# Kernel optimization log

Hardware: AMD Instinct MI355X
Metric: run time of the kernel (lower is better)

Reference implementation:

```python
import jax, jax.numpy as jnp
import numpy as np

N_NODES = 100000
N_EDGES = 3200000

def setup_inputs() -> dict:
    key = jax.random.key(0)
    ks = jax.random.split(key, 6)
    x = jax.random.normal(ks[0], (N_NODES, 128), dtype=jnp.float32)
    edge_index = jax.random.randint(ks[1], (2, N_EDGES), 0, N_NODES, dtype=jnp.int64)
    W1 = jax.random.normal(ks[2], (128, 64), dtype=jnp.float32) * 0.05
    b1 = jnp.zeros((64,), dtype=jnp.float32)
    W2 = jax.random.normal(ks[3], (64, 64), dtype=jnp.float32) * 0.05
    b2 = jnp.zeros((64,), dtype=jnp.float32)
    Wf = jax.random.normal(ks[4], (64, 40), dtype=jnp.float32) * 0.05
    bf = jnp.zeros((40,), dtype=jnp.float32)
    return {"x": x, "edge_index": edge_index, "W1": W1, "b1": b1,
            "W2": W2, "b2": b2, "Wf": Wf, "bf": bf}

def _gcn_graph(edge_index, n_nodes):
    # Add self loops (PyG GCNConv default), compute symmetric norm.
    loop = jnp.arange(n_nodes, dtype=edge_index.dtype)
    src = jnp.concatenate([edge_index[0], loop])
    dst = jnp.concatenate([edge_index[1], loop])
    deg = jax.ops.segment_sum(jnp.ones_like(dst, dtype=jnp.float32), dst,
                              num_segments=n_nodes)
    dinv = jnp.where(deg > 0, jax.lax.rsqrt(deg), 0.0)
    norm = dinv[src] * dinv[dst]  # [E+N]
    return src, dst, norm

def _gcn_layer(x, W, b, src, dst, norm, n_nodes):
    h = x @ W                     # transform first (as PyG GCNConv)
    msg = h[src] * norm[:, None]  # gather + scale
    agg = jax.ops.segment_sum(msg, dst, num_segments=n_nodes)  # scatter-sum
    return agg + b

def reference(x, edge_index, W1, b1, W2, b2, Wf, bf):
    n = x.shape[0]
    src, dst, norm = _gcn_graph(edge_index, n)
    h = jax.nn.relu(_gcn_layer(x, W1, b1, src, dst, norm, n))
    h = jax.nn.relu(_gcn_layer(h, W2, b2, src, dst, norm, n))
    logits = h @ Wf + bf
    return jax.nn.log_softmax(logits, axis=1)
```

## Files before the change

### kernel.cpp

```cpp
#include <hip/hip_runtime.h>
#include <hip/hip_fp16.h>
#include <cstdint>
#include <cstddef>
#include <cmath>


#define T1  4096
#define BSH 7
#define CAP 6144

typedef _Float16 half8 __attribute__((ext_vector_type(8)));
typedef float f32x4 __attribute__((ext_vector_type(4)));
typedef float f32x2 __attribute__((ext_vector_type(2)));

__global__ __launch_bounds__(1024) void k_prep(const float* __restrict__ W1,
        const float* __restrict__ W2, const float* __restrict__ Wf,
        int* __restrict__ cursor1, uint4* __restrict__ W1fr,
        uint4* __restrict__ W2fr, uint4* __restrict__ Wffr, int NB) {
    int t = threadIdx.x;
    for (int i = t; i < NB; i += 1024) cursor1[i] = i * CAP;
    if (t < 64) {
        int r16 = t & 15, kg = t >> 4;
        #pragma unroll
        for (int ct = 0; ct < 4; ++ct)
            #pragma unroll
            for (int kt = 0; kt < 4; ++kt) {
                half8 h;
                #pragma unroll
                for (int j = 0; j < 8; ++j)
                    h[j] = (_Float16)W1[(kt * 32 + kg * 8 + j) * 64 + ct * 16 + r16];
                W1fr[(ct * 4 + kt) * 64 + t] = *(uint4*)&h;
            }
        #pragma unroll
        for (int ct = 0; ct < 4; ++ct)
            #pragma unroll
            for (int kt = 0; kt < 2; ++kt) {
                half8 h;
                #pragma unroll
                for (int j = 0; j < 8; ++j)
                    h[j] = (_Float16)W2[(kt * 32 + kg * 8 + j) * 64 + ct * 16 + r16];
                W2fr[(ct * 2 + kt) * 64 + t] = *(uint4*)&h;
            }
        #pragma unroll
        for (int ct = 0; ct < 3; ++ct)
            #pragma unroll
            for (int kt = 0; kt < 2; ++kt) {
                int col = ct * 16 + r16;
                half8 h;
                #pragma unroll
                for (int j = 0; j < 8; ++j)
                    h[j] = (col < 40) ? (_Float16)Wf[(kt * 32 + kg * 8 + j) * 40 + col]
                                      : (_Float16)0.f;
                Wffr[(ct * 2 + kt) * 64 + t] = *(uint4*)&h;
            }
    }
}

__global__ __launch_bounds__(256) void k_pass1(const int* __restrict__ src,
        const int* __restrict__ dst, int* __restrict__ cursor1,
        unsigned int* __restrict__ tmp, int E, int NB) {
    __shared__ unsigned int pack[T1];
    __shared__ unsigned short bkt[T1];
    __shared__ int h[1024], hs_[1024], gbase[1024];
    __shared__ int wtot[4];
    int t = threadIdx.x;
    for (int i = t; i < 1024; i += 256) h[i] = 0;
    __syncthreads();
    int base = blockIdx.x * T1;
    int n = min(T1, E - base);
    int nv4 = n >> 2, rem = n & 3;
    unsigned int pk[16];
    int bl[16];
    #pragma unroll
    for (int i = 0; i < 4; ++i) {
        int g = i * 256 + t;
        if (g < nv4) {
            int4 s4 = ((const int4*)(src + base))[g];
            int4 d4 = ((const int4*)(dst + base))[g];
            int b0 = d4.x >> BSH;
            pk[4*i]   = (unsigned)s4.x | ((unsigned)(d4.x & 127) << 17);
            bl[4*i]   = (b0 << 13) | atomicAdd(&h[b0], 1);
            int b1 = d4.y >> BSH;
            pk[4*i+1] = (unsigned)s4.y | ((unsigned)(d4.y & 127) << 17);
            bl[4*i+1] = (b1 << 13) | atomicAdd(&h[b1], 1);
            int b2 = d4.z >> BSH;
            pk[4*i+2] = (unsigned)s4.z | ((unsigned)(d4.z & 127) << 17);
            bl[4*i+2] = (b2 << 13) | atomicAdd(&h[b2], 1);
            int b3 = d4.w >> BSH;
            pk[4*i+3] = (unsigned)s4.w | ((unsigned)(d4.w & 127) << 17);
            bl[4*i+3] = (b3 << 13) | atomicAdd(&h[b3], 1);
        } else {
            bl[4*i] = bl[4*i+1] = bl[4*i+2] = bl[4*i+3] = -1;
        }
    }
    unsigned int pk_r = 0; int bl_r = -1;
    if (t < rem) {
        int idx = nv4 * 4 + t;
        int s_ = src[base + idx], d = dst[base + idx];
        int b = d >> BSH;
        pk_r = (unsigned)s_ | ((unsigned)(d & 127) << 17);
        bl_r = (b << 13) | atomicAdd(&h[b], 1);
    }
    __syncthreads();
    {
        int b0 = 4 * t;
        int e0 = h[b0], e1 = h[b0+1], e2 = h[b0+2], e3 = h[b0+3];
        int s1 = e0 + e1, s2 = s1 + e2, s3 = s2 + e3;
        int lane = t & 63, wv = t >> 6;
        int vv = s3;
        #pragma unroll
        for (int o = 1; o < 64; o <<= 1) {
            int u = __shfl_up(vv, o, 64);
            if (lane >= o) vv += u;
        }
        if (lane == 63) wtot[wv] = vv;
        __syncthreads();
        int off = 0;
        #pragma unroll
        for (int w = 0; w < 4; ++w) off += (w < wv) ? wtot[w] : 0;
        int excl = off + vv - s3;
        hs_[b0]   = excl + e0;
        hs_[b0+1] = excl + s1;
        hs_[b0+2] = excl + s2;
        hs_[b0+3] = excl + s3;
    }
    __syncthreads();
    for (int i = t; i < NB; i += 256)
        gbase[i] = h[i] ? atomicAdd(&cursor1[i], h[i]) : 0;
    __syncthreads();
    #pragma unroll
    for (int i = 0; i < 16; ++i) {
        if (bl[i] >= 0) {
            int b = bl[i] >> 13, lo = bl[i] & 8191;
            int slot = hs_[b] - h[b] + lo;
            pack[slot] = pk[i];
            bkt[slot]  = (unsigned short)b;
        }
    }
    if (bl_r >= 0) {
        int b = bl_r >> 13, lo = bl_r & 8191;
        int slot = hs_[b] - h[b] + lo;
        pack[slot] = pk_r;
        bkt[slot]  = (unsigned short)b;
    }
    __syncthreads();
    for (int s_ = t; s_ < n; s_ += 256) {
        int b = bkt[s_];
        tmp[gbase[b] + (s_ - (hs_[b] - h[b]))] = pack[s_];
    }
}

__global__ __launch_bounds__(512) void k_p2x(const unsigned int* __restrict__ tmp,
        const int* __restrict__ cursor1, int2* __restrict__ rcp,
        int* __restrict__ csrc, float* __restrict__ dinv,
        const float* __restrict__ x, const uint4* __restrict__ W1fr,
        unsigned int* __restrict__ hs, int N) {
    __shared__ int c[8][128], cur[8][128];
    __shared__ float sdinv[128];
    __shared__ int wsum;
    int t = threadIdx.x, b = blockIdx.x;
    int wv = t >> 6;
    for (int i = t; i < 1024; i += 512) ((int*)c)[i] = 0;
    __syncthreads();
    int s0 = b * CAP, s1 = cursor1[b];
    int n = s1 - s0;
    int nv4 = n >> 2, rem = n & 3;
    const uint4* tmp4 = (const uint4*)(tmp + s0);
    for (int i = t; i < nv4; i += 512) {
        uint4 v = tmp4[i];
        atomicAdd(&c[wv][(v.x >> 17) & 127], 1);
        atomicAdd(&c[wv][(v.y >> 17) & 127], 1);
        atomicAdd(&c[wv][(v.z >> 17) & 127], 1);
        atomicAdd(&c[wv][(v.w >> 17) & 127], 1);
    }
    if (t < rem)
        atomicAdd(&c[wv][(tmp[s0 + nv4 * 4 + t] >> 17) & 127], 1);
    __syncthreads();
    int totv = 0, vv = 0;
    if (t < 128) {
        #pragma unroll
        for (int w = 0; w < 8; ++w) totv += c[w][t];
        vv = totv;
        #pragma unroll
        for (int o = 1; o < 64; o <<= 1) {
            int u = __shfl_up(vv, o, 64);
            if ((t & 63) >= o) vv += u;
        }
        if (t == 63) wsum = vv;
    }
    __syncthreads();
    if (t < 128) {
        if (t >= 64) vv += wsum;
        int rp = s0 + vv - totv;
        float dv = rsqrtf((float)totv + 1.0f);
        sdinv[t] = dv;
        int node = b * 128 + t;
        if (node < N) {
            rcp[node]  = make_int2(rp, totv);
            dinv[node] = dv;
        }
        int run = rp;
        #pragma unroll
        for (int w = 0; w < 8; ++w) { cur[w][t] = run; run += c[w][t]; }
    }
    __syncthreads();
    for (int i = t; i < nv4; i += 512) {
        uint4 v = tmp4[i];
        int q0 = atomicAdd(&cur[wv][(v.x >> 17) & 127], 1);
        csrc[q0] = (int)(v.x & 0x1FFFFu);
        int q1 = atomicAdd(&cur[wv][(v.y >> 17) & 127], 1);
        csrc[q1] = (int)(v.y & 0x1FFFFu);
        int q2 = atomicAdd(&cur[wv][(v.z >> 17) & 127], 1);
        csrc[q2] = (int)(v.z & 0x1FFFFu);
        int q3 = atomicAdd(&cur[wv][(v.w >> 17) & 127], 1);
        csrc[q3] = (int)(v.w & 0x1FFFFu);
    }
    if (t < rem) {
        unsigned int p = tmp[s0 + nv4 * 4 + t];
        int q = atomicAdd(&cur[wv][(p >> 17) & 127], 1);
        csrc[q] = (int)(p & 0x1FFFFu);
    }
    __syncthreads();
    int lane = t & 63, wid = t >> 6;
    int r16 = lane & 15, kg = lane >> 4;
    half8 bf[4][4];
    #pragma unroll
    for (int ct = 0; ct < 4; ++ct)
        #pragma unroll
        for (int kt = 0; kt < 4; ++kt)
            bf[ct][kt] = *(const half8*)&W1fr[(ct * 4 + kt) * 64 + lane];
    int v0 = b * 128 + wid * 16;
    int rowA = min(v0 + r16, N - 1);
    const float* xp = x + (size_t)rowA * 128 + kg * 8;
    half8 af[4];
    #pragma unroll
    for (int kt = 0; kt < 4; ++kt) {
        float4 p = *(const float4*)(xp + kt * 32);
        float4 q = *(const float4*)(xp + kt * 32 + 4);
        half8 a;
        a[0] = (_Float16)p.x; a[1] = (_Float16)p.y;
        a[2] = (_Float16)p.z; a[3] = (_Float16)p.w;
        a[4] = (_Float16)q.x; a[5] = (_Float16)q.y;
        a[6] = (_Float16)q.z; a[7] = (_Float16)q.w;
        af[kt] = a;
    }
    f32x4 acc0 = {0,0,0,0}, acc1 = {0,0,0,0}, acc2 = {0,0,0,0}, acc3 = {0,0,0,0};
    #pragma unroll
    for (int kt = 0; kt < 4; ++kt) {
        acc0 = __builtin_amdgcn_mfma_f32_16x16x32_f16(af[kt], bf[0][kt], acc0, 0, 0, 0);
        acc1 = __builtin_amdgcn_mfma_f32_16x16x32_f16(af[kt], bf[1][kt], acc1, 0, 0, 0);
        acc2 = __builtin_amdgcn_mfma_f32_16x16x32_f16(af[kt], bf[2][kt], acc2, 0, 0, 0);
        acc3 = __builtin_amdgcn_mfma_f32_16x16x32_f16(af[kt], bf[3][kt], acc3, 0, 0, 0);
    }
    #pragma unroll
    for (int r = 0; r < 4; ++r) {
        int nd = v0 + kg * 4 + r;
        if (nd < N) {
            float d = sdinv[wid * 16 + kg * 4 + r];
            int pk = __builtin_amdgcn_cvt_pk_fp8_f32(d * acc0[r], d * acc1[r], 0, false);
            pk     = __builtin_amdgcn_cvt_pk_fp8_f32(d * acc2[r], d * acc3[r], pk, true);
            hs[((size_t)nd << 4) + r16] = (unsigned int)pk;
        }
    }
}

__global__ __launch_bounds__(256) void k_agg(const int2* __restrict__ rcp,
        const int* __restrict__ csrc, const unsigned int* __restrict__ hp,
        float* __restrict__ acc, int N) {
    int w = (blockIdx.x * 256 + threadIdx.x) >> 6;
    int lane = threadIdx.x & 63;
    if (w >= N) return;
    int grp = lane >> 4, sub = lane & 15;
    int2 rc = rcp[w];
    int rs = rc.x, re = rc.x + rc.y;
    f32x2 A = {0.f, 0.f}, B = {0.f, 0.f};
    if (grp == 0) {
        unsigned v = hp[((size_t)w << 4) + sub];
        A = __builtin_amdgcn_cvt_pk_f32_fp8((int)v, false);
        B = __builtin_amdgcn_cvt_pk_f32_fp8((int)v, true);
    }
    int eb = rs;
    for (; eb + 32 <= re; eb += 32) {
        int e = eb + grp;
        int u0 = csrc[e];      int u1 = csrc[e + 4];
        int u2 = csrc[e + 8];  int u3 = csrc[e + 12];
        int u4 = csrc[e + 16]; int u5 = csrc[e + 20];
        int u6 = csrc[e + 24]; int u7 = csrc[e + 28];
        unsigned v0 = hp[((size_t)u0 << 4) + sub];
        unsigned v1 = hp[((size_t)u1 << 4) + sub];
        unsigned v2 = hp[((size_t)u2 << 4) + sub];
        unsigned v3 = hp[((size_t)u3 << 4) + sub];
        unsigned v4 = hp[((size_t)u4 << 4) + sub];
        unsigned v5 = hp[((size_t)u5 << 4) + sub];
        unsigned v6 = hp[((size_t)u6 << 4) + sub];
        unsigned v7 = hp[((size_t)u7 << 4) + sub];
        A += __builtin_amdgcn_cvt_pk_f32_fp8((int)v0, false);
        B += __builtin_amdgcn_cvt_pk_f32_fp8((int)v0, true);
        A += __builtin_amdgcn_cvt_pk_f32_fp8((int)v1, false);
        B += __builtin_amdgcn_cvt_pk_f32_fp8((int)v1, true);
        A += __builtin_amdgcn_cvt_pk_f32_fp8((int)v2, false);
        B += __builtin_amdgcn_cvt_pk_f32_fp8((int)v2, true);
        A += __builtin_amdgcn_cvt_pk_f32_fp8((int)v3, false);
        B += __builtin_amdgcn_cvt_pk_f32_fp8((int)v3, true);
        A += __builtin_amdgcn_cvt_pk_f32_fp8((int)v4, false);
        B += __builtin_amdgcn_cvt_pk_f32_fp8((int)v4, true);
        A += __builtin_amdgcn_cvt_pk_f32_fp8((int)v5, false);
        B += __builtin_amdgcn_cvt_pk_f32_fp8((int)v5, true);
        A += __builtin_amdgcn_cvt_pk_f32_fp8((int)v6, false);
        B += __builtin_amdgcn_cvt_pk_f32_fp8((int)v6, true);
        A += __builtin_amdgcn_cvt_pk_f32_fp8((int)v7, false);
        B += __builtin_amdgcn_cvt_pk_f32_fp8((int)v7, true);
    }
    int e = eb + grp;
    if (e < re) {
        int e1 = min(e + 4,  re - 1);
        int e2 = min(e + 8,  re - 1);
        int e3 = min(e + 12, re - 1);
        int e4 = min(e + 16, re - 1);
        int e5 = min(e + 20, re - 1);
        int e6 = min(e + 24, re - 1);
        int e7 = min(e + 28, re - 1);
        int u0 = csrc[e];
        int u1 = csrc[e1];
        int u2 = csrc[e2];
        int u3 = csrc[e3];
        int u4 = csrc[e4];
        int u5 = csrc[e5];
        int u6 = csrc[e6];
        int u7 = csrc[e7];
        unsigned v0 = hp[((size_t)u0 << 4) + sub];
        unsigned v1 = hp[((size_t)u1 << 4) + sub];
        unsigned v2 = hp[((size_t)u2 << 4) + sub];
        unsigned v3 = hp[((size_t)u3 << 4) + sub];
        unsigned v4 = hp[((size_t)u4 << 4) + sub];
        unsigned v5 = hp[((size_t)u5 << 4) + sub];
        unsigned v6 = hp[((size_t)u6 << 4) + sub];
        unsigned v7 = hp[((size_t)u7 << 4) + sub];
        float m1 = (e + 4  < re) ? 1.f : 0.f;
        float m2 = (e + 8  < re) ? 1.f : 0.f;
        float m3 = (e + 12 < re) ? 1.f : 0.f;
        float m4 = (e + 16 < re) ? 1.f : 0.f;
        float m5 = (e + 20 < re) ? 1.f : 0.f;
        float m6 = (e + 24 < re) ? 1.f : 0.f;
        float m7 = (e + 28 < re) ? 1.f : 0.f;
        A += __builtin_amdgcn_cvt_pk_f32_fp8((int)v0, false);
        B += __builtin_amdgcn_cvt_pk_f32_fp8((int)v0, true);
        f32x2 M1 = {m1, m1}, M2 = {m2, m2}, M3 = {m3, m3};
        f32x2 M4 = {m4, m4}, M5 = {m5, m5}, M6 = {m6, m6}, M7 = {m7, m7};
        A += M1 * __builtin_amdgcn_cvt_pk_f32_fp8((int)v1, false);
        B += M1 * __builtin_amdgcn_cvt_pk_f32_fp8((int)v1, true);
        A += M2 * __builtin_amdgcn_cvt_pk_f32_fp8((int)v2, false);
        B += M2 * __builtin_amdgcn_cvt_pk_f32_fp8((int)v2, true);
        A += M3 * __builtin_amdgcn_cvt_pk_f32_fp8((int)v3, false);
        B += M3 * __builtin_amdgcn_cvt_pk_f32_fp8((int)v3, true);
        A += M4 * __builtin_amdgcn_cvt_pk_f32_fp8((int)v4, false);
        B += M4 * __builtin_amdgcn_cvt_pk_f32_fp8((int)v4, true);
        A += M5 * __builtin_amdgcn_cvt_pk_f32_fp8((int)v5, false);
        B += M5 * __builtin_amdgcn_cvt_pk_f32_fp8((int)v5, true);
        A += M6 * __builtin_amdgcn_cvt_pk_f32_fp8((int)v6, false);
        B += M6 * __builtin_amdgcn_cvt_pk_f32_fp8((int)v6, true);
        A += M7 * __builtin_amdgcn_cvt_pk_f32_fp8((int)v7, false);
        B += M7 * __builtin_amdgcn_cvt_pk_f32_fp8((int)v7, true);
    }
    float a0 = A[0], a1 = A[1], a2 = B[0], a3 = B[1];
    a0 += __shfl_xor(a0, 16, 64); a0 += __shfl_xor(a0, 32, 64);
    a1 += __shfl_xor(a1, 16, 64); a1 += __shfl_xor(a1, 32, 64);
    a2 += __shfl_xor(a2, 16, 64); a2 += __shfl_xor(a2, 32, 64);
    a3 += __shfl_xor(a3, 16, 64); a3 += __shfl_xor(a3, 32, 64);
    if (grp == 0) {
        float* op = acc + ((size_t)w << 6) + sub;
        op[0]  = a0;
        op[16] = a1;
        op[32] = a2;
        op[48] = a3;
    }
}

__global__ __launch_bounds__(256) void k_xform2(const float* __restrict__ acc_in,
        const uint4* __restrict__ W2fr, const float* __restrict__ b1,
        const float* __restrict__ dinv, unsigned int* __restrict__ hs2, int N, int ntiles) {
    int t = threadIdx.x;
    int lane = t & 63, wid = t >> 6;
    int r16 = lane & 15, kg = lane >> 4;
    half8 bf[4][2];
    #pragma unroll
    for (int ct = 0; ct < 4; ++ct)
        #pragma unroll
        for (int kt = 0; kt < 2; ++kt)
            bf[ct][kt] = *(const half8*)&W2fr[(ct * 2 + kt) * 64 + lane];
    float b1r[2][8];
    #pragma unroll
    for (int kt = 0; kt < 2; ++kt)
        #pragma unroll
        for (int j = 0; j < 8; ++j) b1r[kt][j] = b1[kt * 32 + kg * 8 + j];
    int wtile = blockIdx.x * 4 + wid;
    int nw = gridDim.x * 4;
    for (int tile = wtile; tile < ntiles; tile += nw) {
        int v0 = tile * 16;
        int rowA = min(v0 + r16, N - 1);
        float da = dinv[rowA];
        const float* ap = acc_in + ((size_t)rowA << 6) + kg * 8;
        half8 af[2];
        #pragma unroll
        for (int kt = 0; kt < 2; ++kt) {
            float4 p = *(const float4*)(ap + kt * 32);
            float4 q = *(const float4*)(ap + kt * 32 + 4);
            half8 a;
            a[0] = (_Float16)fmaxf(fmaf(da, p.x, b1r[kt][0]), 0.f);
            a[1] = (_Float16)fmaxf(fmaf(da, p.y, b1r[kt][1]), 0.f);
            a[2] = (_Float16)fmaxf(fmaf(da, p.z, b1r[kt][2]), 0.f);
            a[3] = (_Float16)fmaxf(fmaf(da, p.w, b1r[kt][3]), 0.f);
            a[4] = (_Float16)fmaxf(fmaf(da, q.x, b1r[kt][4]), 0.f);
            a[5] = (_Float16)fmaxf(fmaf(da, q.y, b1r[kt][5]), 0.f);
            a[6] = (_Float16)fmaxf(fmaf(da, q.z, b1r[kt][6]), 0.f);
            a[7] = (_Float16)fmaxf(fmaf(da, q.w, b1r[kt][7]), 0.f);
            af[kt] = a;
        }
        f32x4 acc0 = {0,0,0,0}, acc1 = {0,0,0,0}, acc2 = {0,0,0,0}, acc3 = {0,0,0,0};
        #pragma unroll
        for (int kt = 0; kt < 2; ++kt) {
            acc0 = __builtin_amdgcn_mfma_f32_16x16x32_f16(af[kt], bf[0][kt], acc0, 0, 0, 0);
            acc1 = __builtin_amdgcn_mfma_f32_16x16x32_f16(af[kt], bf[1][kt], acc1, 0, 0, 0);
            acc2 = __builtin_amdgcn_mfma_f32_16x16x32_f16(af[kt], bf[2][kt], acc2, 0, 0, 0);
            acc3 = __builtin_amdgcn_mfma_f32_16x16x32_f16(af[kt], bf[3][kt], acc3, 0, 0, 0);
        }
        #pragma unroll
        for (int r = 0; r < 4; ++r) {
            int node = v0 + kg * 4 + r;
            if (node < N) {
                float d = dinv[node];
                int pk = __builtin_amdgcn_cvt_pk_fp8_f32(d * acc0[r], d * acc1[r], 0, false);
                pk     = __builtin_amdgcn_cvt_pk_fp8_f32(d * acc2[r], d * acc3[r], pk, true);
                hs2[((size_t)node << 4) + r16] = (unsigned int)pk;
            }
        }
    }
}

__global__ __launch_bounds__(256) void k_final(const float* __restrict__ acc2,
        const uint4* __restrict__ Wffr, const float* __restrict__ b2,
        const float* __restrict__ bf, const float* __restrict__ dinv,
        float* __restrict__ out, int N, int ntiles) {
    int t = threadIdx.x;
    int lane = t & 63, wid = t >> 6;
    int r16 = lane & 15, kg = lane >> 4;
    half8 bfr[3][2];
    #pragma unroll
    for (int ct = 0; ct < 3; ++ct)
        #pragma unroll
        for (int kt = 0; kt < 2; ++kt)
            bfr[ct][kt] = *(const half8*)&Wffr[(ct * 2 + kt) * 64 + lane];
    float b2r[2][8];
    #pragma unroll
    for (int kt = 0; kt < 2; ++kt)
        #pragma unroll
        for (int j = 0; j < 8; ++j) b2r[kt][j] = b2[kt * 32 + kg * 8 + j];
    float bf0 = bf[r16];
    float bf1 = bf[16 + r16];
    float bf2 = (r16 < 8) ? bf[32 + r16] : 0.f;
    int wtile = blockIdx.x * 4 + wid;
    int nw = gridDim.x * 4;
    for (int tile = wtile; tile < ntiles; tile += nw) {
        int v0 = tile * 16;
        int rowA = min(v0 + r16, N - 1);
        float da = dinv[rowA];
        const float* ap = acc2 + ((size_t)rowA << 6) + kg * 8;
        half8 af[2];
        #pragma unroll
        for (int kt = 0; kt < 2; ++kt) {
            float4 p = *(const float4*)(ap + kt * 32);
            float4 q = *(const float4*)(ap + kt * 32 + 4);
            half8 a;
            a[0] = (_Float16)fmaxf(fmaf(da, p.x, b2r[kt][0]), 0.f);
            a[1] = (_Float16)fmaxf(fmaf(da, p.y, b2r[kt][1]), 0.f);
            a[2] = (_Float16)fmaxf(fmaf(da, p.z, b2r[kt][2]), 0.f);
            a[3] = (_Float16)fmaxf(fmaf(da, p.w, b2r[kt][3]), 0.f);
            a[4] = (_Float16)fmaxf(fmaf(da, q.x, b2r[kt][4]), 0.f);
            a[5] = (_Float16)fmaxf(fmaf(da, q.y, b2r[kt][5]), 0.f);
            a[6] = (_Float16)fmaxf(fmaf(da, q.z, b2r[kt][6]), 0.f);
            a[7] = (_Float16)fmaxf(fmaf(da, q.w, b2r[kt][7]), 0.f);
            af[kt] = a;
        }
        f32x4 a0 = {0,0,0,0}, a1 = {0,0,0,0}, a2 = {0,0,0,0};
        #pragma unroll
        for (int kt = 0; kt < 2; ++kt) {
            a0 = __builtin_amdgcn_mfma_f32_16x16x32_f16(af[kt], bfr[0][kt], a0, 0, 0, 0);
            a1 = __builtin_amdgcn_mfma_f32_16x16x32_f16(af[kt], bfr[1][kt], a1, 0, 0, 0);
            a2 = __builtin_amdgcn_mfma_f32_16x16x32_f16(af[kt], bfr[2][kt], a2, 0, 0, 0);
        }
        #pragma unroll
        for (int r = 0; r < 4; ++r) {
            float z0 = a0[r] + bf0;
            float z1 = a1[r] + bf1;
            float z2 = (r16 < 8) ? (a2[r] + bf2) : -INFINITY;
            float m = fmaxf(fmaxf(z0, z1), z2);
            #pragma unroll
            for (int o = 8; o; o >>= 1) m = fmaxf(m, __shfl_xor(m, o, 64));
            float s = expf(z0 - m) + expf(z1 - m) + ((r16 < 8) ? expf(z2 - m) : 0.f);
            #pragma unroll
            for (int o = 8; o; o >>= 1) s += __shfl_xor(s, o, 64);
            float ls = m + logf(s);
            int node = v0 + kg * 4 + r;
            if (node < N) {
                float* op = out + (size_t)node * 40;
                op[r16]      = z0 - ls;
                op[16 + r16] = z1 - ls;
                if (r16 < 8) op[32 + r16] = z2 - ls;
            }
        }
    }
}

extern "C" void kernel_launch(void* const* d_in, const int* in_sizes, int n_in,
                              void* d_out, int out_size, void* d_ws, size_t ws_size,
                              hipStream_t stream) {
    const float* x  = (const float*)d_in[0];
    const int*   ei = (const int*)d_in[1];
    const float* W1 = (const float*)d_in[2];
    const float* b1 = (const float*)d_in[3];
    const float* W2 = (const float*)d_in[4];
    const float* b2 = (const float*)d_in[5];
    const float* Wf = (const float*)d_in[6];
    const float* bf = (const float*)d_in[7];
    float* out = (float*)d_out;

    const int N = in_sizes[0] / 128;
    const int E = in_sizes[1] / 2;
    const int* src = ei;
    const int* dst = ei + E;
    const int NB = (N + 127) >> BSH;

    auto align = [](size_t s) { return (s + 255) & ~(size_t)255; };
    char* ws = (char*)d_ws;
    size_t o = 0;
    int2*  rcp     = (int2*)(ws + o);  o += align((size_t)N * 8);
    float* dinv    = (float*)(ws + o); o += align((size_t)N * 4);
    int*   cursor1 = (int*)(ws + o);   o += align(1024 * 4);
    uint4* W1fr    = (uint4*)(ws + o); o += align(16 * 64 * 16);
    uint4* W2fr    = (uint4*)(ws + o); o += align(8 * 64 * 16);
    uint4* Wffr    = (uint4*)(ws + o); o += align(6 * 64 * 16);
    int*   csrc    = (int*)(ws + o);   o += align((size_t)NB * CAP * 4);
    unsigned int* B1 = (unsigned int*)(ws + o); o += align((size_t)N * 64);
    float*  B2     = (float*)(ws + o);  o += align((size_t)N * 64 * 4);
    unsigned int* tmp = (unsigned int*)B2;

    int blkT  = (E + T1 - 1) / T1;
    int ntile = (N + 15) / 16;
    int gX = 512;

    k_prep <<<1,   1024, 0, stream>>>(W1, W2, Wf, cursor1, W1fr, W2fr, Wffr, NB);
    k_pass1<<<blkT, 256, 0, stream>>>(src, dst, cursor1, tmp, E, NB);
    k_p2x  <<<NB,   512, 0, stream>>>(tmp, cursor1, rcp, csrc, dinv, x, W1fr, B1, N);

    int blkAgg = (N * 64 + 255) / 256;
    k_agg   <<<blkAgg, 256, 0, stream>>>(rcp, csrc, B1, B2, N);
    k_xform2<<<gX, 256, 0, stream>>>(B2, W2fr, b1, dinv, B1, N, ntile);
    k_agg   <<<blkAgg, 256, 0, stream>>>(rcp, csrc, B1, B2, N);
    k_final <<<gX, 256, 0, stream>>>(B2, Wffr, b2, bf, dinv, out, N, ntile);
}
```

Before: 185.0 us.

## Drop weight-prep kernel, convert weights inline, and widen pass1 blocks

Removes the single-block k_prep kernel. Each MFMA kernel now builds its fp16 weight fragments directly from the fp32 weights, and the bucket cursors are cleared with a memset and offset by i*CAP at use. The goal is to cut a serial launch and a dependency step from the pipeline. k_pass1 also moves from 256 to 512 threads per block, with the scan changed to two buckets per thread. In exchange, every block now does strided uncoalesced weight reads and conversions, and a memset is added.

```diff
diff --git a/kernel.cpp b/kernel.cpp
--- a/kernel.cpp
+++ b/kernel.cpp
@@ -13,67 +13,24 @@
 typedef float f32x4 __attribute__((ext_vector_type(4)));
 typedef float f32x2 __attribute__((ext_vector_type(2)));
 
-__global__ __launch_bounds__(1024) void k_prep(const float* __restrict__ W1,
-        const float* __restrict__ W2, const float* __restrict__ Wf,
-        int* __restrict__ cursor1, uint4* __restrict__ W1fr,
-        uint4* __restrict__ W2fr, uint4* __restrict__ Wffr, int NB) {
-    int t = threadIdx.x;
-    for (int i = t; i < NB; i += 1024) cursor1[i] = i * CAP;
-    if (t < 64) {
-        int r16 = t & 15, kg = t >> 4;
-        #pragma unroll
-        for (int ct = 0; ct < 4; ++ct)
-            #pragma unroll
-            for (int kt = 0; kt < 4; ++kt) {
-                half8 h;
-                #pragma unroll
-                for (int j = 0; j < 8; ++j)
-                    h[j] = (_Float16)W1[(kt * 32 + kg * 8 + j) * 64 + ct * 16 + r16];
-                W1fr[(ct * 4 + kt) * 64 + t] = *(uint4*)&h;
-            }
-        #pragma unroll
-        for (int ct = 0; ct < 4; ++ct)
-            #pragma unroll
-            for (int kt = 0; kt < 2; ++kt) {
-                half8 h;
-                #pragma unroll
-                for (int j = 0; j < 8; ++j)
-                    h[j] = (_Float16)W2[(kt * 32 + kg * 8 + j) * 64 + ct * 16 + r16];
-                W2fr[(ct * 2 + kt) * 64 + t] = *(uint4*)&h;
-            }
-        #pragma unroll
-        for (int ct = 0; ct < 3; ++ct)
-            #pragma unroll
-            for (int kt = 0; kt < 2; ++kt) {
-                int col = ct * 16 + r16;
-                half8 h;
-                #pragma unroll
-                for (int j = 0; j < 8; ++j)
-                    h[j] = (col < 40) ? (_Float16)Wf[(kt * 32 + kg * 8 + j) * 40 + col]
-                                      : (_Float16)0.f;
-                Wffr[(ct * 2 + kt) * 64 + t] = *(uint4*)&h;
-            }
-    }
-}
-
-__global__ __launch_bounds__(256) void k_pass1(const int* __restrict__ src,
+__global__ __launch_bounds__(512) void k_pass1(const int* __restrict__ src,
         const int* __restrict__ dst, int* __restrict__ cursor1,
         unsigned int* __restrict__ tmp, int E, int NB) {
     __shared__ unsigned int pack[T1];
     __shared__ unsigned short bkt[T1];
     __shared__ int h[1024], hs_[1024], gbase[1024];
-    __shared__ int wtot[4];
+    __shared__ int wtot[8];
     int t = threadIdx.x;
-    for (int i = t; i < 1024; i += 256) h[i] = 0;
+    for (int i = t; i < 1024; i += 512) h[i] = 0;
     __syncthreads();
     int base = blockIdx.x * T1;
     int n = min(T1, E - base);
     int nv4 = n >> 2, rem = n & 3;
-    unsigned int pk[16];
-    int bl[16];
-    #pragma unroll
-    for (int i = 0; i < 4; ++i) {
-        int g = i * 256 + t;
+    unsigned int pk[8];
+    int bl[8];
+    #pragma unroll
+    for (int i = 0; i < 2; ++i) {
+        int g = i * 512 + t;
         if (g < nv4) {
             int4 s4 = ((const int4*)(src + base))[g];
             int4 d4 = ((const int4*)(dst + base))[g];
@@ -103,11 +60,11 @@
     }
     __syncthreads();
     {
-        int b0 = 4 * t;
-        int e0 = h[b0], e1 = h[b0+1], e2 = h[b0+2], e3 = h[b0+3];
-        int s1 = e0 + e1, s2 = s1 + e2, s3 = s2 + e3;
+        int b0 = 2 * t;
+        int e0 = h[b0], e1 = h[b0 + 1];
+        int sum2 = e0 + e1;
         int lane = t & 63, wv = t >> 6;
-        int vv = s3;
+        int vv = sum2;
         #pragma unroll
         for (int o = 1; o < 64; o <<= 1) {
             int u = __shfl_up(vv, o, 64);
@@ -117,19 +74,17 @@
         __syncthreads();
         int off = 0;
         #pragma unroll
-        for (int w = 0; w < 4; ++w) off += (w < wv) ? wtot[w] : 0;
-        int excl = off + vv - s3;
-        hs_[b0]   = excl + e0;
-        hs_[b0+1] = excl + s1;
-        hs_[b0+2] = excl + s2;
-        hs_[b0+3] = excl + s3;
-    }
-    __syncthreads();
-    for (int i = t; i < NB; i += 256)
-        gbase[i] = h[i] ? atomicAdd(&cursor1[i], h[i]) : 0;
-    __syncthreads();
-    #pragma unroll
-    for (int i = 0; i < 16; ++i) {
+        for (int w = 0; w < 8; ++w) off += (w < wv) ? wtot[w] : 0;
+        int excl = off + vv - sum2;
+        hs_[b0]     = excl + e0;
+        hs_[b0 + 1] = excl + sum2;
+    }
+    __syncthreads();
+    for (int i = t; i < NB; i += 512)
+        gbase[i] = h[i] ? (i * CAP + atomicAdd(&cursor1[i], h[i])) : 0;
+    __syncthreads();
+    #pragma unroll
+    for (int i = 0; i < 8; ++i) {
         if (bl[i] >= 0) {
             int b = bl[i] >> 13, lo = bl[i] & 8191;
             int slot = hs_[b] - h[b] + lo;
@@ -144,7 +99,7 @@
         bkt[slot]  = (unsigned short)b;
     }
     __syncthreads();
-    for (int s_ = t; s_ < n; s_ += 256) {
+    for (int s_ = t; s_ < n; s_ += 512) {
         int b = bkt[s_];
         tmp[gbase[b] + (s_ - (hs_[b] - h[b]))] = pack[s_];
     }
@@ -153,7 +108,7 @@
 __global__ __launch_bounds__(512) void k_p2x(const unsigned int* __restrict__ tmp,
         const int* __restrict__ cursor1, int2* __restrict__ rcp,
         int* __restrict__ csrc, float* __restrict__ dinv,
-        const float* __restrict__ x, const uint4* __restrict__ W1fr,
+        const float* __restrict__ x, const float* __restrict__ W1,
         unsigned int* __restrict__ hs, int N) {
     __shared__ int c[8][128], cur[8][128];
     __shared__ float sdinv[128];
@@ -162,8 +117,8 @@
     int wv = t >> 6;
     for (int i = t; i < 1024; i += 512) ((int*)c)[i] = 0;
     __syncthreads();
-    int s0 = b * CAP, s1 = cursor1[b];
-    int n = s1 - s0;
+    int s0 = b * CAP;
+    int n = cursor1[b];
     int nv4 = n >> 2, rem = n & 3;
     const uint4* tmp4 = (const uint4*)(tmp + s0);
     for (int i = t; i < nv4; i += 512) {
@@ -227,8 +182,13 @@
     #pragma unroll
     for (int ct = 0; ct < 4; ++ct)
         #pragma unroll
-        for (int kt = 0; kt < 4; ++kt)
-            bf[ct][kt] = *(const half8*)&W1fr[(ct * 4 + kt) * 64 + lane];
+        for (int kt = 0; kt < 4; ++kt) {
+            const float* wp = W1 + (kt * 32 + kg * 8) * 64 + ct * 16 + r16;
+            half8 h;
+            #pragma unroll
+            for (int j = 0; j < 8; ++j) h[j] = (_Float16)wp[j * 64];
+            bf[ct][kt] = h;
+        }
     int v0 = b * 128 + wid * 16;
     int rowA = min(v0 + r16, N - 1);
     const float* xp = x + (size_t)rowA * 128 + kg * 8;
@@ -377,7 +337,7 @@
 }
 
 __global__ __launch_bounds__(256) void k_xform2(const float* __restrict__ acc_in,
-        const uint4* __restrict__ W2fr, const float* __restrict__ b1,
+        const float* __restrict__ W2, const float* __restrict__ b1,
         const float* __restrict__ dinv, unsigned int* __restrict__ hs2, int N, int ntiles) {
     int t = threadIdx.x;
     int lane = t & 63, wid = t >> 6;
@@ -386,8 +346,13 @@
     #pragma unroll
     for (int ct = 0; ct < 4; ++ct)
         #pragma unroll
-        for (int kt = 0; kt < 2; ++kt)
-            bf[ct][kt] = *(const half8*)&W2fr[(ct * 2 + kt) * 64 + lane];
+        for (int kt = 0; kt < 2; ++kt) {
+            const float* wp = W2 + (kt * 32 + kg * 8) * 64 + ct * 16 + r16;
+            half8 h;
+            #pragma unroll
+            for (int j = 0; j < 8; ++j) h[j] = (_Float16)wp[j * 64];
+            bf[ct][kt] = h;
+        }
     float b1r[2][8];
     #pragma unroll
     for (int kt = 0; kt < 2; ++kt)
@@ -438,7 +403,7 @@
 }
 
 __global__ __launch_bounds__(256) void k_final(const float* __restrict__ acc2,
-        const uint4* __restrict__ Wffr, const float* __restrict__ b2,
+        const float* __restrict__ Wf, const float* __restrict__ b2,
         const float* __restrict__ bf, const float* __restrict__ dinv,
         float* __restrict__ out, int N, int ntiles) {
     int t = threadIdx.x;
@@ -448,8 +413,16 @@
     #pragma unroll
     for (int ct = 0; ct < 3; ++ct)
         #pragma unroll
-        for (int kt = 0; kt < 2; ++kt)
-            bfr[ct][kt] = *(const half8*)&Wffr[(ct * 2 + kt) * 64 + lane];
+        for (int kt = 0; kt < 2; ++kt) {
+            int col = ct * 16 + r16;
+            half8 h;
+            #pragma unroll
+            for (int j = 0; j < 8; ++j) {
+                int k = kt * 32 + kg * 8 + j;
+                h[j] = (col < 40) ? (_Float16)Wf[k * 40 + col] : (_Float16)0.f;
+            }
+            bfr[ct][kt] = h;
+        }
     float b2r[2][8];
     #pragma unroll
     for (int kt = 0; kt < 2; ++kt)
@@ -536,25 +509,23 @@
     int2*  rcp     = (int2*)(ws + o);  o += align((size_t)N * 8);
     float* dinv    = (float*)(ws + o); o += align((size_t)N * 4);
     int*   cursor1 = (int*)(ws + o);   o += align(1024 * 4);
-    uint4* W1fr    = (uint4*)(ws + o); o += align(16 * 64 * 16);
-    uint4* W2fr    = (uint4*)(ws + o); o += align(8 * 64 * 16);
-    uint4* Wffr    = (uint4*)(ws + o); o += align(6 * 64 * 16);
     int*   csrc    = (int*)(ws + o);   o += align((size_t)NB * CAP * 4);
     unsigned int* B1 = (unsigned int*)(ws + o); o += align((size_t)N * 64);
     float*  B2     = (float*)(ws + o);  o += align((size_t)N * 64 * 4);
     unsigned int* tmp = (unsigned int*)B2;
 
+    hipMemsetAsync(cursor1, 0, (size_t)NB * 4, stream);
+
     int blkT  = (E + T1 - 1) / T1;
     int ntile = (N + 15) / 16;
     int gX = 512;
 
-    k_prep <<<1,   1024, 0, stream>>>(W1, W2, Wf, cursor1, W1fr, W2fr, Wffr, NB);
-    k_pass1<<<blkT, 256, 0, stream>>>(src, dst, cursor1, tmp, E, NB);
-    k_p2x  <<<NB,   512, 0, stream>>>(tmp, cursor1, rcp, csrc, dinv, x, W1fr, B1, N);
+    k_pass1<<<blkT, 512, 0, stream>>>(src, dst, cursor1, tmp, E, NB);
+    k_p2x  <<<NB,   512, 0, stream>>>(tmp, cursor1, rcp, csrc, dinv, x, W1, B1, N);
 
     int blkAgg = (N * 64 + 255) / 256;
     k_agg   <<<blkAgg, 256, 0, stream>>>(rcp, csrc, B1, B2, N);
-    k_xform2<<<gX, 256, 0, stream>>>(B2, W2fr, b1, dinv, B1, N, ntile);
+    k_xform2<<<gX, 256, 0, stream>>>(B2, W2, b1, dinv, B1, N, ntile);
     k_agg   <<<blkAgg, 256, 0, stream>>>(rcp, csrc, B1, B2, N);
-    k_final <<<gX, 256, 0, stream>>>(B2, Wffr, b2, bf, dinv, out, N, ntile);
+    k_final <<<gX, 256, 0, stream>>>(B2, Wf, b2, bf, dinv, out, N, ntile);
 }
```

Result: no change. 181.4 us (-2.0%).
